# Kernel tuning notes

Measured on AMD Instinct MI355X. Metric: run time of the kernel, lower is better.

The kernel has to match this reference:

```python
import jax, jax.numpy as jnp
import numpy as np

B, S, D, H, DH, TLEN, TD = 4, 1024, 1024, 16, 64, 256, 256
EPS = 1e-5


def layer_norm(x, g, b):
    m = jnp.mean(x, axis=-1, keepdims=True)
    v = jnp.mean((x - m) ** 2, axis=-1, keepdims=True)
    return (x - m) * jax.lax.rsqrt(v + EPS) * g + b


def rotate_half(x):
    x1, x2 = jnp.split(x, 2, axis=-1)
    return jnp.concatenate((-x2, x1), axis=-1)


def apply_rope(pos, t):
    # pos: [S, DH] -> [1, S, 1, DH]; t: [B, S, H, DH]
    p = pos[None, :, None, :]
    return t * jnp.cos(p) + rotate_half(t) * jnp.sin(p)


def mha(q_in, kv_in, in_w, in_b, out_w, out_b, n_heads):
    # standard nn.MultiheadAttention math (batch-first tensors here)
    d = q_in.shape[-1]
    dh = d // n_heads
    q = q_in @ in_w[:d].T + in_b[:d]
    k = kv_in @ in_w[d:2 * d].T + in_b[d:2 * d]
    v = kv_in @ in_w[2 * d:].T + in_b[2 * d:]
    q = q.reshape(q.shape[0], q.shape[1], n_heads, dh)
    k = k.reshape(k.shape[0], k.shape[1], n_heads, dh)
    v = v.reshape(v.shape[0], v.shape[1], n_heads, dh)
    scores = jnp.einsum('bihd,bjhd->bhij', q, k) / jnp.sqrt(jnp.asarray(dh, q.dtype))
    attn = jax.nn.softmax(scores, axis=-1)
    o = jnp.einsum('bhij,bjhd->bihd', attn, v)
    o = o.reshape(o.shape[0], o.shape[1], d)
    return o @ out_w.T + out_b


def setup_inputs():
    key = jax.random.key(0)
    ks = jax.random.split(key, 20)
    s = 0.02
    inp = {
        'x': jax.random.normal(ks[0], (B, S, D), jnp.float32),
        'text_emb': jax.random.normal(ks[1], (B, TLEN, D), jnp.float32),
        'time_emb': jax.random.normal(ks[2], (B, TD), jnp.float32),
    }
    # true RoPE position encoding, matching RotaryEmbedding.forward
    inv_freq = 1.0 / (10000 ** (jnp.arange(0, DH, 2, dtype=jnp.float32) / DH))
    freqs = jnp.arange(S, dtype=jnp.float32)[:, None] * inv_freq[None, :]
    inp['rotary_pos'] = jnp.concatenate((freqs, freqs), axis=-1)  # [S, DH]
    inp.update(
        ln1_g=jnp.ones((D,), jnp.float32), ln1_b=jnp.zeros((D,), jnp.float32),
        ln2_g=jnp.ones((D,), jnp.float32), ln2_b=jnp.zeros((D,), jnp.float32),
        ln3_g=jnp.ones((D,), jnp.float32), ln3_b=jnp.zeros((D,), jnp.float32),
        attn_in_w=jax.random.normal(ks[3], (3 * D, D), jnp.float32) * s,
        attn_in_b=jnp.zeros((3 * D,), jnp.float32),
        ca_in_w=jax.random.normal(ks[4], (3 * D, D), jnp.float32) * s,
        ca_in_b=jnp.zeros((3 * D,), jnp.float32),
        ca_out_w=jax.random.normal(ks[5], (D, D), jnp.float32) * s,
        ca_out_b=jnp.zeros((D,), jnp.float32),
        fc1_w=jax.random.normal(ks[6], (4 * D, D), jnp.float32) * s,
        fc1_b=jnp.zeros((4 * D,), jnp.float32),
        gate_w=jax.random.normal(ks[7], (4 * D, D), jnp.float32) * s,
        gate_b=jnp.zeros((4 * D,), jnp.float32),
        fc2_w=jax.random.normal(ks[8], (D, 4 * D), jnp.float32) * s,
        fc2_b=jnp.zeros((D,), jnp.float32),
    )
    return inp


def reference(x, text_emb, time_emb, rotary_pos,
              ln1_g, ln1_b, ln2_g, ln2_b, ln3_g, ln3_b,
              attn_in_w, attn_in_b,
              ca_in_w, ca_in_b, ca_out_w, ca_out_b,
              fc1_w, fc1_b, gate_w, gate_b, fc2_w, fc2_b):
    b, n, d = x.shape
    # --- self-attention with manual RoPE (NOTE: original skips out_proj) ---
    residual = x
    xn = layer_norm(x, ln1_g, ln1_b)
    q = xn @ attn_in_w[:d].T + attn_in_b[:d]
    k = xn @ attn_in_w[d:2 * d].T + attn_in_b[d:2 * d]
    v = xn @ attn_in_w[2 * d:].T + attn_in_b[2 * d:]
    q = q.reshape(b, n, H, DH)
    k = k.reshape(b, n, H, DH)
    v = v.reshape(b, n, H, DH)
    q = apply_rope(rotary_pos, q)
    k = apply_rope(rotary_pos, k)
    scores = jnp.einsum('bihd,bjhd->bhij', q, k) / jnp.sqrt(jnp.asarray(DH, x.dtype))
    attn = jax.nn.softmax(scores, axis=-1)
    attn_out = jnp.einsum('bhij,bjhd->bihd', attn, v).reshape(b, n, d)
    x = attn_out + residual
    # --- cross-attention (full MHA, dropout inactive at eval) ---
    residual = x
    xn = layer_norm(x, ln2_g, ln2_b)
    x = mha(xn, text_emb, ca_in_w, ca_in_b, ca_out_w, ca_out_b, H) + residual
    # --- gated MLP ---
    residual = x
    xn = layer_norm(x, ln3_g, ln3_b)
    h = jax.nn.gelu(xn @ fc1_w.T + fc1_b, approximate=False)
    g = jax.nn.sigmoid(xn @ gate_w.T + gate_b)
    return (h * g) @ fc2_w.T + fc2_b + residual
```

## Files before the change

kernel.cpp:

```cpp
#include <hip/hip_runtime.h>
#include <hip/hip_bf16.h>

#define SEQ 1024
#define DIM 1024
#define NH 16

typedef __bf16 bf16_t;
typedef __bf16 bf16x8 __attribute__((ext_vector_type(8)));
typedef __bf16 bf16x4 __attribute__((ext_vector_type(4)));
typedef float f32x4 __attribute__((ext_vector_type(4)));

__device__ __forceinline__ f32x4 mfma16(bf16x8 a, bf16x8 b, f32x4 c) {
    return __builtin_amdgcn_mfma_f32_16x16x32_bf16(a, b, c, 0, 0, 0);
}

__device__ __forceinline__ void gload16(const bf16_t* g, bf16_t* l) {
    __builtin_amdgcn_global_load_lds(
        (const __attribute__((address_space(1))) void*)g,
        (__attribute__((address_space(3))) void*)l, 16, 0, 0);
}

enum { EPI_BF16 = 0, EPI_F32_RESID = 1 };

__global__ __launch_bounds__(256) void cvt_kernel(const float* __restrict__ in,
                                                  bf16_t* __restrict__ out) {
    const int i = blockIdx.x * 256 + threadIdx.x;
    const float4 v = ((const float4*)in)[i];
    bf16x4 o = {(bf16_t)v.x, (bf16_t)v.y, (bf16_t)v.z, (bf16_t)v.w};
    ((bf16x4*)out)[i] = o;
}

__global__ __launch_bounds__(256) void ln_kernel(const float* __restrict__ in,
                                                 const float* __restrict__ g,
                                                 const float* __restrict__ bsh,
                                                 bf16_t* __restrict__ out) {
    __shared__ float red[4], red2[4];
    const int row = blockIdx.x, tid = threadIdx.x;
    const float4 v = ((const float4*)(in + (size_t)row * DIM))[tid];
    float s = v.x + v.y + v.z + v.w;
#pragma unroll
    for (int o = 32; o; o >>= 1) s += __shfl_down(s, o, 64);
    if ((tid & 63) == 0) red[tid >> 6] = s;
    __syncthreads();
    const float mean = (red[0] + red[1] + red[2] + red[3]) * (1.0f / DIM);
    const float dx = v.x - mean, dy = v.y - mean, dz = v.z - mean, dw = v.w - mean;
    float s2 = dx * dx + dy * dy + dz * dz + dw * dw;
#pragma unroll
    for (int o = 32; o; o >>= 1) s2 += __shfl_xor(s2, o, 64);
    if ((tid & 63) == 0) red2[tid >> 6] = s2;
    __syncthreads();
    const float var = (red2[0] + red2[1] + red2[2] + red2[3]) * (1.0f / DIM);
    const float rs = rsqrtf(var + 1e-5f);
    const float4 gv = ((const float4*)g)[tid];
    const float4 bv = ((const float4*)bsh)[tid];
    bf16x4 o4 = {(bf16_t)(dx * rs * gv.x + bv.x), (bf16_t)(dy * rs * gv.y + bv.y),
                 (bf16_t)(dz * rs * gv.z + bv.z), (bf16_t)(dw * rs * gv.w + bv.w)};
    ((bf16x4*)(out + (size_t)row * DIM))[tid] = o4;
}

__global__ __launch_bounds__(256) void rope_kernel(bf16_t* __restrict__ qkv,
                                                   const float* __restrict__ rp) {
    const int t = blockIdx.x * 256 + threadIdx.x;
    const int row = t >> 9;
    const int rem = t & 511;
    const int h = rem >> 5, d = rem & 31;
    const int s = row & (SEQ - 1);
    const float p0 = rp[s * 64 + d];
    const float p1 = rp[s * 64 + d + 32];
    float s0, c0, s1, c1;
    sincosf(p0, &s0, &c0);
    sincosf(p1, &s1, &c1);
    const size_t base = (size_t)row * 3072 + h * 64 + d;
#pragma unroll
    for (int off = 0; off <= 1024; off += 1024) {
        const float a = (float)qkv[base + off];
        const float b = (float)qkv[base + off + 32];
        qkv[base + off] = (bf16_t)(a * c0 - b * s0);
        qkv[base + off + 32] = (bf16_t)(b * c1 + a * s1);
    }
}

__device__ __forceinline__ float epi_apply_gelu(float v) {
    return 0.5f * v * (1.0f + erff(v * 0.70710678118f));
}

__global__ __launch_bounds__(256) void vtrans_kernel(
    const bf16_t* __restrict__ src, int ld, int voff, int skv,
    bf16_t* __restrict__ vt) {
    __shared__ bf16_t T[64 * 72];
    const int qt = blockIdx.x, h = blockIdx.y, b = blockIdx.z;
    const int tid = threadIdx.x;
    const int s0 = qt * 64;
#pragma unroll
    for (int t = 0; t < 2; ++t) {
        const int idx = t * 256 + tid;
        const int r = idx >> 3, c8 = (idx & 7) * 8;
        bf16x8 v = *(const bf16x8*)(src + (size_t)(b * skv + s0 + r) * ld +
                                    voff + h * 64 + c8);
        *(bf16x8*)&T[r * 72 + c8] = v;
    }
    __syncthreads();
    const size_t base = ((size_t)(b * NH + h) * 64) * skv;
#pragma unroll
    for (int t = 0; t < 2; ++t) {
        const int idx = t * 256 + tid;
        const int d = idx >> 3, s8 = (idx & 7) * 8;
        bf16x8 w;
#pragma unroll
        for (int i = 0; i < 8; ++i) w[i] = T[(s8 + i) * 72 + d];
        *(bf16x8*)(vt + base + (size_t)d * skv + s0 + s8) = w;
    }
}

#define ALD 72
template <bool OUTBF>
__global__ __launch_bounds__(256) void attn2_kernel(
    const bf16_t* __restrict__ qp, int ldq, int qoff,
    const bf16_t* __restrict__ kp, int ldk, int koff,
    const bf16_t* __restrict__ vtp, int skv,
    const float* __restrict__ resid, void* __restrict__ outp, float scale) {
    __shared__ bf16_t Ks[4096];
    __shared__ bf16_t Vs[4096];
    __shared__ bf16_t Ps[4 * 16 * ALD];
    const int nwg = gridDim.x;
    const int t = (blockIdx.x & 7) * (nwg >> 3) + (blockIdx.x >> 3);
    const int qt = t & 15;
    const int bh = t >> 4;
    const int b = bh >> 4, h = bh & 15;
    const int tid = threadIdx.x;
    const int wave = tid >> 6, lane = tid & 63;
    const int lr = lane & 15, hi = lane >> 4;

    const size_t qrow = (size_t)(b * SEQ + qt * 64 + wave * 16 + lr);
    const bf16_t* qb = qp + qrow * ldq + qoff + h * 64;
    const bf16x8 qf0 = *(const bf16x8*)(qb + hi * 8);
    const bf16x8 qf1 = *(const bf16x8*)(qb + 32 + hi * 8);

    const bf16_t* vbase = vtp + ((size_t)bh * 64) * skv;

    f32x4 oacc[4];
#pragma unroll
    for (int n = 0; n < 4; ++n) oacc[n] = (f32x4){0.f, 0.f, 0.f, 0.f};
    float mrun[4] = {-1e30f, -1e30f, -1e30f, -1e30f};
    float lrun[4] = {0.f, 0.f, 0.f, 0.f};

    bf16_t* pw = &Ps[wave * 16 * ALD];
    const int nkt = skv >> 6;
    for (int kt = 0; kt < nkt; ++kt) {
#pragma unroll
        for (int u = 0; u < 2; ++u) {
            const int c = wave * 2 + u;
            const int grow = wave * 16 + lr, gcol = u * 32 + hi * 8;
            gload16(kp + (size_t)(b * skv + kt * 64 + grow) * ldk + koff +
                        h * 64 + gcol,
                    &Ks[c * 512]);
            gload16(vbase + (size_t)grow * skv + kt * 64 + gcol, &Vs[c * 512]);
        }
        __syncthreads();

        f32x4 s[4];
#pragma unroll
        for (int n = 0; n < 4; ++n) {
            f32x4 z = (f32x4){0.f, 0.f, 0.f, 0.f};
            z = mfma16(qf0, *(const bf16x8*)&Ks[(n * 2 + 0) * 512 + hi * 128 + lr * 8], z);
            z = mfma16(qf1, *(const bf16x8*)&Ks[(n * 2 + 1) * 512 + hi * 128 + lr * 8], z);
            s[n] = z * scale;
        }
        float alpha[4];
#pragma unroll
        for (int j = 0; j < 4; ++j) {
            float mt = fmaxf(fmaxf(s[0][j], s[1][j]), fmaxf(s[2][j], s[3][j]));
#pragma unroll
            for (int o = 8; o >= 1; o >>= 1) mt = fmaxf(mt, __shfl_xor(mt, o, 64));
            const float mnew = fmaxf(mrun[j], mt);
            alpha[j] = __expf(mrun[j] - mnew);
            float rsum = 0.f;
#pragma unroll
            for (int n = 0; n < 4; ++n) {
                const float p = __expf(s[n][j] - mnew);
                s[n][j] = p;
                rsum += p;
            }
#pragma unroll
            for (int o = 8; o >= 1; o >>= 1) rsum += __shfl_xor(rsum, o, 64);
            lrun[j] = lrun[j] * alpha[j] + rsum;
            mrun[j] = mnew;
        }
#pragma unroll
        for (int j = 0; j < 4; ++j) {
            const int pr = hi * 4 + j;
#pragma unroll
            for (int n = 0; n < 4; ++n) pw[pr * ALD + n * 16 + lr] = (bf16_t)s[n][j];
        }
#pragma unroll
        for (int n = 0; n < 4; ++n)
#pragma unroll
            for (int j = 0; j < 4; ++j) oacc[n][j] *= alpha[j];
#pragma unroll
        for (int ks = 0; ks < 2; ++ks) {
            const bf16x8 pa = *(const bf16x8*)&pw[lr * ALD + ks * 32 + hi * 8];
#pragma unroll
            for (int n = 0; n < 4; ++n) {
                const bf16x8 vf =
                    *(const bf16x8*)&Vs[(n * 2 + ks) * 512 + hi * 128 + lr * 8];
                oacc[n] = mfma16(pa, vf, oacc[n]);
            }
        }
        __syncthreads();
    }

    const size_t orow0 = (size_t)(b * SEQ + qt * 64 + wave * 16);
#pragma unroll
    for (int n = 0; n < 4; ++n) {
#pragma unroll
        for (int j = 0; j < 4; ++j) {
            const int r = hi * 4 + j;
            const size_t idx = (orow0 + r) * DIM + h * 64 + n * 16 + lr;
            float val = oacc[n][j] / lrun[j];
            if constexpr (OUTBF) {
                ((bf16_t*)outp)[idx] = (bf16_t)val;
            } else {
                ((float*)outp)[idx] = val + resid[idx];
            }
        }
    }
}

template <int EPI, int MODE>
__global__ __launch_bounds__(256, 3) void gemm4w(
    const bf16_t* __restrict__ A, int lda, const bf16_t* __restrict__ W, int ldw,
    const float* __restrict__ bias, const void* __restrict__ aux,
    void* __restrict__ outv, int ldo, int K, int nM) {
    __shared__ bf16_t As[2][4096];
    __shared__ bf16_t Bs[2][4096];
    const int tid = threadIdx.x;
    const int wave = tid >> 6, lane = tid & 63;
    const int wm = wave >> 1, wn = wave & 1;
    const int lr = lane & 15, hi = lane >> 4;

    const int x = blockIdx.x & 7, i = blockIdx.x >> 3;
    int mt, nt;
    if constexpr (MODE == 0) {
        const int mc = nM >> 3;
        mt = x * mc + (i % mc);
        nt = i / mc;
    } else {
        const int nc = (gridDim.x / nM) >> 3;
        nt = x * nc + (i % nc);
        mt = i / nc;
    }
    const int rowA0 = mt * 128, rowB0 = nt * 128;

    f32x4 acc[4][4];
#pragma unroll
    for (int m = 0; m < 4; ++m)
#pragma unroll
        for (int n = 0; n < 4; ++n) acc[m][n] = (f32x4){0.f, 0.f, 0.f, 0.f};

    auto stage = [&](int kt, int b) {
        const int k0 = kt * 32;
        const int gcol = k0 + hi * 8;
#pragma unroll
        for (int u = 0; u < 2; ++u) {
            const int c = wave * 2 + u;
            const int grow = c * 16 + lr;
            gload16(A + (size_t)(rowA0 + grow) * lda + gcol, &As[b][c * 512]);
            gload16(W + (size_t)(rowB0 + grow) * ldw + gcol, &Bs[b][c * 512]);
        }
    };

    const int NT = K >> 5;
    stage(0, 0);
    stage(1, 1);
    asm volatile("s_waitcnt vmcnt(4)" ::: "memory");
    __builtin_amdgcn_s_barrier();

    for (int kt = 0; kt < NT; ++kt) {
        const int cur = kt & 1;
        bf16x8 af[4], bfr[4];
#pragma unroll
        for (int mf = 0; mf < 4; ++mf)
            af[mf] = *(const bf16x8*)&As[cur][(wm * 4 + mf) * 512 + hi * 128 + lr * 8];
#pragma unroll
        for (int nf = 0; nf < 4; ++nf)
            bfr[nf] = *(const bf16x8*)&Bs[cur][(wn * 4 + nf) * 512 + hi * 128 + lr * 8];
#pragma unroll
        for (int mf = 0; mf < 4; ++mf)
#pragma unroll
            for (int nf = 0; nf < 4; ++nf)
                acc[mf][nf] = mfma16(af[mf], bfr[nf], acc[mf][nf]);
        if (kt + 1 < NT) {
            __builtin_amdgcn_sched_barrier(0);
            __builtin_amdgcn_s_barrier();
            if (kt + 2 < NT) {
                stage(kt + 2, cur);
                asm volatile("s_waitcnt vmcnt(4)" ::: "memory");
            } else {
                asm volatile("s_waitcnt vmcnt(0)" ::: "memory");
            }
            __builtin_amdgcn_s_barrier();
        }
    }

    float bn[4];
#pragma unroll
    for (int n = 0; n < 4; ++n) bn[n] = bias[rowB0 + wn * 64 + n * 16 + lr];
#pragma unroll
    for (int m = 0; m < 4; ++m) {
#pragma unroll
        for (int j = 0; j < 4; ++j) {
            const int row = rowA0 + wm * 64 + m * 16 + hi * 4 + j;
#pragma unroll
            for (int n = 0; n < 4; ++n) {
                const int col = rowB0 + wn * 64 + n * 16 + lr;
                float val = acc[m][n][j] + bn[n];
                const size_t oidx = (size_t)row * ldo + col;
                if constexpr (EPI == EPI_BF16) {
                    ((bf16_t*)outv)[oidx] = (bf16_t)val;
                } else {
                    ((float*)outv)[oidx] = val + ((const float*)aux)[oidx];
                }
            }
        }
    }
}

__global__ __launch_bounds__(256, 3) void gemm_mlp(
    const bf16_t* __restrict__ A, int lda, const bf16_t* __restrict__ W1,
    const bf16_t* __restrict__ Wg, int ldw, const float* __restrict__ b1,
    const float* __restrict__ bg, bf16_t* __restrict__ outv, int ldo, int K,
    int nM) {
    __shared__ __align__(16) char smem[32768];
    auto As = (bf16_t(*)[4096])smem;
    auto Bs = (bf16_t(*)[4096])(smem + 16384);
    float* gx = (float*)smem;
    const int tid = threadIdx.x;
    const int wave = tid >> 6, lane = tid & 63;
    const int role = wave >> 1, wm = wave & 1;
    const int lr = lane & 15, hi = lane >> 4;

    const int x = blockIdx.x & 7, i = blockIdx.x >> 3;
    const int nc = (gridDim.x / nM) >> 3;
    const int nt = x * nc + (i % nc), mt = i / nc;
    const int rowA0 = mt * 128, colB0 = nt * 64;

    f32x4 acc[4][4];
#pragma unroll
    for (int m = 0; m < 4; ++m)
#pragma unroll
        for (int n = 0; n < 4; ++n) acc[m][n] = (f32x4){0.f, 0.f, 0.f, 0.f};

    auto stage = [&](int kt, int b) {
        const int k0 = kt * 32;
        const int gcol = k0 + hi * 8;
#pragma unroll
        for (int u = 0; u < 2; ++u) {
            const int c = wave * 2 + u;
            gload16(A + (size_t)(rowA0 + c * 16 + lr) * lda + gcol, &As[b][c * 512]);
            const bf16_t* Wsrc = (c < 4) ? W1 : Wg;
            const int wrow = colB0 + (c & 3) * 16 + lr;
            gload16(Wsrc + (size_t)wrow * ldw + gcol, &Bs[b][c * 512]);
        }
    };

    const int NT = K >> 5;
    stage(0, 0);
    stage(1, 1);
    asm volatile("s_waitcnt vmcnt(4)" ::: "memory");
    __builtin_amdgcn_s_barrier();

    for (int kt = 0; kt < NT; ++kt) {
        const int cur = kt & 1;
        bf16x8 af[4], bfr[4];
#pragma unroll
        for (int mf = 0; mf < 4; ++mf)
            af[mf] = *(const bf16x8*)&As[cur][(wm * 4 + mf) * 512 + hi * 128 + lr * 8];
#pragma unroll
        for (int nf = 0; nf < 4; ++nf)
            bfr[nf] = *(const bf16x8*)&Bs[cur][(role * 4 + nf) * 512 + hi * 128 + lr * 8];
#pragma unroll
        for (int mf = 0; mf < 4; ++mf)
#pragma unroll
            for (int nf = 0; nf < 4; ++nf)
                acc[mf][nf] = mfma16(af[mf], bfr[nf], acc[mf][nf]);
        if (kt + 1 < NT) {
            __builtin_amdgcn_sched_barrier(0);
            __builtin_amdgcn_s_barrier();
            if (kt + 2 < NT) {
                stage(kt + 2, cur);
                asm volatile("s_waitcnt vmcnt(4)" ::: "memory");
            } else {
                asm volatile("s_waitcnt vmcnt(0)" ::: "memory");
            }
            __builtin_amdgcn_s_barrier();
        }
    }

    __syncthreads();
    if (role == 1) {
#pragma unroll
        for (int m = 0; m < 4; ++m)
#pragma unroll
            for (int j = 0; j < 4; ++j) {
                const int r = wm * 64 + m * 16 + hi * 4 + j;
#pragma unroll
                for (int n = 0; n < 4; ++n)
                    gx[r * 64 + n * 16 + lr] =
                        acc[m][n][j] + bg[colB0 + n * 16 + lr];
            }
    }
    __syncthreads();
    if (role == 0) {
#pragma unroll
        for (int m = 0; m < 4; ++m) {
#pragma unroll
            for (int j = 0; j < 4; ++j) {
                const int r = wm * 64 + m * 16 + hi * 4 + j;
                const int row = rowA0 + r;
#pragma unroll
                for (int n = 0; n < 4; ++n) {
                    const int col = colB0 + n * 16 + lr;
                    const float h = acc[m][n][j] + b1[col];
                    const float g = gx[r * 64 + n * 16 + lr];
                    const float sg = 1.0f / (1.0f + __expf(-g));
                    outv[(size_t)row * ldo + col] = (bf16_t)(epi_apply_gelu(h) * sg);
                }
            }
        }
    }
}

extern "C" void kernel_launch(void* const* d_in, const int* in_sizes, int n_in,
                              void* d_out, int out_size, void* d_ws, size_t ws_size,
                              hipStream_t stream) {
    const float* x = (const float*)d_in[0];
    const float* text_emb = (const float*)d_in[1];
    const float* rotary = (const float*)d_in[3];
    const float* ln1_g = (const float*)d_in[4];
    const float* ln1_b = (const float*)d_in[5];
    const float* ln2_g = (const float*)d_in[6];
    const float* ln2_b = (const float*)d_in[7];
    const float* ln3_g = (const float*)d_in[8];
    const float* ln3_b = (const float*)d_in[9];
    const float* attn_in_w = (const float*)d_in[10];
    const float* attn_in_b = (const float*)d_in[11];
    const float* ca_in_w = (const float*)d_in[12];
    const float* ca_in_b = (const float*)d_in[13];
    const float* ca_out_w = (const float*)d_in[14];
    const float* ca_out_b = (const float*)d_in[15];
    const float* fc1_w = (const float*)d_in[16];
    const float* fc1_b = (const float*)d_in[17];
    const float* gate_w = (const float*)d_in[18];
    const float* gate_b = (const float*)d_in[19];
    const float* fc2_w = (const float*)d_in[20];
    const float* fc2_b = (const float*)d_in[21];

    char* ws = (char*)d_ws;
    bf16_t* attn_w_bf = (bf16_t*)(ws);
    bf16_t* ca_in_bf = (bf16_t*)(ws + 6291456);
    bf16_t* ca_out_bf = (bf16_t*)(ws + 12582912);
    bf16_t* fc1_bf = (bf16_t*)(ws + 14680064);
    bf16_t* gate_bf = (bf16_t*)(ws + 23068672);
    bf16_t* fc2_bf = (bf16_t*)(ws + 31457280);
    bf16_t* text_bf = (bf16_t*)(ws + 39845888);
    bf16_t* xn = (bf16_t*)(ws + 41943040);
    float* xA = (float*)(ws + 50331648);
    char* S = ws + 67108864;
    bf16_t* qkv = (bf16_t*)S;
    bf16_t* vtSelf = (bf16_t*)(S + 25165824);
    bf16_t* cq = (bf16_t*)S;
    bf16_t* ckv = (bf16_t*)(S + 8388608);
    bf16_t* ca_attn = (bf16_t*)(S + 12582912);
    bf16_t* vtCross = (bf16_t*)(S + 20971520);
    bf16_t* hbuf = (bf16_t*)S;
    float* out = (float*)d_out;

    cvt_kernel<<<3072, 256, 0, stream>>>(attn_in_w, attn_w_bf);
    cvt_kernel<<<3072, 256, 0, stream>>>(ca_in_w, ca_in_bf);
    cvt_kernel<<<1024, 256, 0, stream>>>(ca_out_w, ca_out_bf);
    cvt_kernel<<<4096, 256, 0, stream>>>(fc1_w, fc1_bf);
    cvt_kernel<<<4096, 256, 0, stream>>>(gate_w, gate_bf);
    cvt_kernel<<<4096, 256, 0, stream>>>(fc2_w, fc2_bf);
    cvt_kernel<<<1024, 256, 0, stream>>>(text_emb, text_bf);

    ln_kernel<<<4096, 256, 0, stream>>>(x, ln1_g, ln1_b, xn);
    gemm4w<EPI_BF16, 0><<<768, 256, 0, stream>>>(
        xn, 1024, attn_w_bf, 1024, attn_in_b, nullptr, qkv, 3072, 1024, 32);
    rope_kernel<<<8192, 256, 0, stream>>>(qkv, rotary);
    vtrans_kernel<<<dim3(16, 16, 4), 256, 0, stream>>>(qkv, 3072, 2048, 1024, vtSelf);
    attn2_kernel<false><<<1024, 256, 0, stream>>>(
        qkv, 3072, 0, qkv, 3072, 1024, vtSelf, 1024, x, xA, 0.125f);

    ln_kernel<<<4096, 256, 0, stream>>>(xA, ln2_g, ln2_b, xn);
    gemm4w<EPI_BF16, 0><<<256, 256, 0, stream>>>(
        xn, 1024, ca_in_bf, 1024, ca_in_b, nullptr, cq, 1024, 1024, 32);
    gemm4w<EPI_BF16, 1><<<128, 256, 0, stream>>>(
        text_bf, 1024, ca_in_bf + (size_t)1024 * 1024, 1024, ca_in_b + 1024, nullptr,
        ckv, 2048, 1024, 8);
    vtrans_kernel<<<dim3(4, 16, 4), 256, 0, stream>>>(ckv, 2048, 1024, 256, vtCross);
    attn2_kernel<true><<<1024, 256, 0, stream>>>(
        cq, 1024, 0, ckv, 2048, 0, vtCross, 256, nullptr, ca_attn, 0.125f);
    gemm4w<EPI_F32_RESID, 0><<<256, 256, 0, stream>>>(
        ca_attn, 1024, ca_out_bf, 1024, ca_out_b, xA, xA, 1024, 1024, 32);

    ln_kernel<<<4096, 256, 0, stream>>>(xA, ln3_g, ln3_b, xn);
    gemm_mlp<<<2048, 256, 0, stream>>>(
        xn, 1024, fc1_bf, gate_bf, 1024, fc1_b, gate_b, hbuf, 4096, 1024, 32);
    gemm4w<EPI_F32_RESID, 0><<<256, 256, 0, stream>>>(
        hbuf, 4096, fc2_bf, 4096, fc2_b, xA, out, 1024, 4096, 32);
}
```

Before: 527.6 us.

## Add 256x256-tile 8-wave GEMM and use it for QKV and MLP projections

Introduces a 512-thread GEMM kernel with 256x256 output tiles, BK=64 double-buffered LDS staging, and an MFMA schedule split into four quadrants, with interleaved barriers and setprio. It replaces the QKV projection GEMM and splits the fused fc1/gate GEMM into two launches: a GELU epilogue, then a sigmoid-multiply epilogue that reads the stored bf16 h back in place. The larger tiles are meant to raise arithmetic intensity and cut global traffic per FLOP. In exchange, the MLP path writes and re-reads the hidden buffer, h is rounded to bf16 before the multiply, and the grids get smaller (192/256 blocks), which may leave CUs underused.

```diff
diff --git a/kernel.cpp b/kernel.cpp
--- a/kernel.cpp
+++ b/kernel.cpp
@@ -20,7 +20,7 @@
         (__attribute__((address_space(3))) void*)l, 16, 0, 0);
 }
 
-enum { EPI_BF16 = 0, EPI_F32_RESID = 1 };
+enum { EPI_BF16 = 0, EPI_F32_RESID = 1, EPI_BF16_GELU = 2, EPI_BF16_SIGMUL = 3 };
 
 __global__ __launch_bounds__(256) void cvt_kernel(const float* __restrict__ in,
                                                   bf16_t* __restrict__ out) {
@@ -226,6 +226,175 @@
     }
 }
 
+template <int EPI>
+__global__ __launch_bounds__(512, 2) void gemm8p(
+    const bf16_t* __restrict__ A, int lda, const bf16_t* __restrict__ W, int ldw,
+    const float* __restrict__ bias, const void* __restrict__ aux,
+    void* __restrict__ outv, int ldo, int K, int nM) {
+    __shared__ bf16_t As[2][16384];
+    __shared__ bf16_t Bs[2][16384];
+    const int tid = threadIdx.x;
+    const int wave = tid >> 6, lane = tid & 63;
+    const int wm = wave >> 2, wn = wave & 3;
+    const int lr = lane & 15, hi = lane >> 4;
+
+    const int x = blockIdx.x & 7, i = blockIdx.x >> 3;
+    const int mc = nM >> 3;
+    const int mt = x * mc + (i % mc);
+    const int nt = i / mc;
+    const int rowA0 = mt * 256, rowB0 = nt * 256;
+
+    f32x4 acc[8][4];
+#pragma unroll
+    for (int m = 0; m < 8; ++m)
+#pragma unroll
+        for (int n = 0; n < 4; ++n) acc[m][n] = (f32x4){0.f, 0.f, 0.f, 0.f};
+
+    auto stageA = [&](int kt, int b) {
+        const int k0 = kt * 64;
+#pragma unroll
+        for (int h2 = 0; h2 < 2; ++h2)
+#pragma unroll
+            for (int u = 0; u < 2; ++u) {
+                const int c = wave * 2 + u;
+                const int grow = rowA0 + h2 * 128 + (c >> 1) * 16 + lr;
+                const int gcol = k0 + (c & 1) * 32 + hi * 8;
+                gload16(A + (size_t)grow * lda + gcol, &As[b][h2 * 8192 + c * 512]);
+            }
+    };
+    auto stageB = [&](int kt, int b) {
+        const int k0 = kt * 64;
+#pragma unroll
+        for (int h2 = 0; h2 < 2; ++h2)
+#pragma unroll
+            for (int u = 0; u < 2; ++u) {
+                const int c = wave * 2 + u;
+                const int grow = rowB0 + h2 * 128 + (c >> 1) * 16 + lr;
+                const int gcol = k0 + (c & 1) * 32 + hi * 8;
+                gload16(W + (size_t)grow * ldw + gcol, &Bs[b][h2 * 8192 + c * 512]);
+            }
+    };
+
+    const int NT = K >> 6;
+    stageA(0, 0);
+    stageB(0, 0);
+    stageA(1, 1);
+    stageB(1, 1);
+    asm volatile("s_waitcnt vmcnt(8)" ::: "memory");
+    __builtin_amdgcn_s_barrier();
+
+    for (int kt = 0; kt < NT; ++kt) {
+        const int cur = kt & 1;
+        const bf16_t* Ab = &As[cur][wm * 8192];
+        const bf16_t* Bb = &Bs[cur][(wn >> 1) * 8192 + (wn & 1) * 4096];
+        bf16x8 af[4][2], bflo[2][2], bfhi[2][2];
+
+#pragma unroll
+        for (int mf = 0; mf < 4; ++mf)
+#pragma unroll
+            for (int ks = 0; ks < 2; ++ks)
+                af[mf][ks] = *(const bf16x8*)&Ab[(mf * 2 + ks) * 512 + lane * 8];
+#pragma unroll
+        for (int nf = 0; nf < 2; ++nf)
+#pragma unroll
+            for (int ks = 0; ks < 2; ++ks)
+                bflo[nf][ks] = *(const bf16x8*)&Bb[(nf * 2 + ks) * 512 + lane * 8];
+        __builtin_amdgcn_s_barrier();
+        __builtin_amdgcn_s_setprio(1);
+#pragma unroll
+        for (int mf = 0; mf < 4; ++mf)
+#pragma unroll
+            for (int nf = 0; nf < 2; ++nf)
+#pragma unroll
+                for (int ks = 0; ks < 2; ++ks)
+                    acc[mf][nf] = mfma16(af[mf][ks], bflo[nf][ks], acc[mf][nf]);
+        __builtin_amdgcn_s_setprio(0);
+        __builtin_amdgcn_s_barrier();
+
+#pragma unroll
+        for (int nf = 0; nf < 2; ++nf)
+#pragma unroll
+            for (int ks = 0; ks < 2; ++ks)
+                bfhi[nf][ks] = *(const bf16x8*)&Bb[((nf + 2) * 2 + ks) * 512 + lane * 8];
+        __builtin_amdgcn_s_barrier();
+        __builtin_amdgcn_s_setprio(1);
+#pragma unroll
+        for (int mf = 0; mf < 4; ++mf)
+#pragma unroll
+            for (int nf = 0; nf < 2; ++nf)
+#pragma unroll
+                for (int ks = 0; ks < 2; ++ks)
+                    acc[mf][nf + 2] = mfma16(af[mf][ks], bfhi[nf][ks], acc[mf][nf + 2]);
+        __builtin_amdgcn_s_setprio(0);
+        __builtin_amdgcn_s_barrier();
+
+#pragma unroll
+        for (int mf = 0; mf < 4; ++mf)
+#pragma unroll
+            for (int ks = 0; ks < 2; ++ks)
+                af[mf][ks] = *(const bf16x8*)&Ab[((mf + 4) * 2 + ks) * 512 + lane * 8];
+        if (kt + 2 < NT) stageB(kt + 2, cur);
+        __builtin_amdgcn_s_barrier();
+        __builtin_amdgcn_s_setprio(1);
+#pragma unroll
+        for (int mf = 0; mf < 4; ++mf)
+#pragma unroll
+            for (int nf = 0; nf < 2; ++nf)
+#pragma unroll
+                for (int ks = 0; ks < 2; ++ks)
+                    acc[mf + 4][nf + 2] = mfma16(af[mf][ks], bfhi[nf][ks], acc[mf + 4][nf + 2]);
+        __builtin_amdgcn_s_setprio(0);
+        __builtin_amdgcn_s_barrier();
+
+        if (kt + 2 < NT) stageA(kt + 2, cur);
+        __builtin_amdgcn_s_barrier();
+        __builtin_amdgcn_s_setprio(1);
+#pragma unroll
+        for (int mf = 0; mf < 4; ++mf)
+#pragma unroll
+            for (int nf = 0; nf < 2; ++nf)
+#pragma unroll
+                for (int ks = 0; ks < 2; ++ks)
+                    acc[mf + 4][nf] = mfma16(af[mf][ks], bflo[nf][ks], acc[mf + 4][nf]);
+        __builtin_amdgcn_s_setprio(0);
+        if (kt + 1 < NT) {
+            if (kt + 2 < NT)
+                asm volatile("s_waitcnt vmcnt(8)" ::: "memory");
+            else
+                asm volatile("s_waitcnt vmcnt(0)" ::: "memory");
+            __builtin_amdgcn_s_barrier();
+        }
+    }
+
+    float bn[4];
+#pragma unroll
+    for (int n = 0; n < 4; ++n) bn[n] = bias[rowB0 + wn * 64 + n * 16 + lr];
+#pragma unroll
+    for (int m = 0; m < 8; ++m) {
+#pragma unroll
+        for (int j = 0; j < 4; ++j) {
+            const int row = rowA0 + wm * 128 + m * 16 + hi * 4 + j;
+#pragma unroll
+            for (int n = 0; n < 4; ++n) {
+                const int col = rowB0 + wn * 64 + n * 16 + lr;
+                float val = acc[m][n][j] + bn[n];
+                const size_t oidx = (size_t)row * ldo + col;
+                if constexpr (EPI == EPI_BF16) {
+                    ((bf16_t*)outv)[oidx] = (bf16_t)val;
+                } else if constexpr (EPI == EPI_BF16_GELU) {
+                    ((bf16_t*)outv)[oidx] = (bf16_t)epi_apply_gelu(val);
+                } else if constexpr (EPI == EPI_BF16_SIGMUL) {
+                    const float sg = 1.0f / (1.0f + __expf(-val));
+                    ((bf16_t*)outv)[oidx] =
+                        (bf16_t)(sg * (float)((const bf16_t*)aux)[oidx]);
+                } else {
+                    ((float*)outv)[oidx] = val + ((const float*)aux)[oidx];
+                }
+            }
+        }
+    }
+}
+
 template <int EPI, int MODE>
 __global__ __launch_bounds__(256, 3) void gemm4w(
     const bf16_t* __restrict__ A, int lda, const bf16_t* __restrict__ W, int ldw,
@@ -319,111 +488,6 @@
                     ((bf16_t*)outv)[oidx] = (bf16_t)val;
                 } else {
                     ((float*)outv)[oidx] = val + ((const float*)aux)[oidx];
-                }
-            }
-        }
-    }
-}
-
-__global__ __launch_bounds__(256, 3) void gemm_mlp(
-    const bf16_t* __restrict__ A, int lda, const bf16_t* __restrict__ W1,
-    const bf16_t* __restrict__ Wg, int ldw, const float* __restrict__ b1,
-    const float* __restrict__ bg, bf16_t* __restrict__ outv, int ldo, int K,
-    int nM) {
-    __shared__ __align__(16) char smem[32768];
-    auto As = (bf16_t(*)[4096])smem;
-    auto Bs = (bf16_t(*)[4096])(smem + 16384);
-    float* gx = (float*)smem;
-    const int tid = threadIdx.x;
-    const int wave = tid >> 6, lane = tid & 63;
-    const int role = wave >> 1, wm = wave & 1;
-    const int lr = lane & 15, hi = lane >> 4;
-
-    const int x = blockIdx.x & 7, i = blockIdx.x >> 3;
-    const int nc = (gridDim.x / nM) >> 3;
-    const int nt = x * nc + (i % nc), mt = i / nc;
-    const int rowA0 = mt * 128, colB0 = nt * 64;
-
-    f32x4 acc[4][4];
-#pragma unroll
-    for (int m = 0; m < 4; ++m)
-#pragma unroll
-        for (int n = 0; n < 4; ++n) acc[m][n] = (f32x4){0.f, 0.f, 0.f, 0.f};
-
-    auto stage = [&](int kt, int b) {
-        const int k0 = kt * 32;
-        const int gcol = k0 + hi * 8;
-#pragma unroll
-        for (int u = 0; u < 2; ++u) {
-            const int c = wave * 2 + u;
-            gload16(A + (size_t)(rowA0 + c * 16 + lr) * lda + gcol, &As[b][c * 512]);
-            const bf16_t* Wsrc = (c < 4) ? W1 : Wg;
-            const int wrow = colB0 + (c & 3) * 16 + lr;
-            gload16(Wsrc + (size_t)wrow * ldw + gcol, &Bs[b][c * 512]);
-        }
-    };
-
-    const int NT = K >> 5;
-    stage(0, 0);
-    stage(1, 1);
-    asm volatile("s_waitcnt vmcnt(4)" ::: "memory");
-    __builtin_amdgcn_s_barrier();
-
-    for (int kt = 0; kt < NT; ++kt) {
-        const int cur = kt & 1;
-        bf16x8 af[4], bfr[4];
-#pragma unroll
-        for (int mf = 0; mf < 4; ++mf)
-            af[mf] = *(const bf16x8*)&As[cur][(wm * 4 + mf) * 512 + hi * 128 + lr * 8];
-#pragma unroll
-        for (int nf = 0; nf < 4; ++nf)
-            bfr[nf] = *(const bf16x8*)&Bs[cur][(role * 4 + nf) * 512 + hi * 128 + lr * 8];
-#pragma unroll
-        for (int mf = 0; mf < 4; ++mf)
-#pragma unroll
-            for (int nf = 0; nf < 4; ++nf)
-                acc[mf][nf] = mfma16(af[mf], bfr[nf], acc[mf][nf]);
-        if (kt + 1 < NT) {
-            __builtin_amdgcn_sched_barrier(0);
-            __builtin_amdgcn_s_barrier();
-            if (kt + 2 < NT) {
-                stage(kt + 2, cur);
-                asm volatile("s_waitcnt vmcnt(4)" ::: "memory");
-            } else {
-                asm volatile("s_waitcnt vmcnt(0)" ::: "memory");
-            }
-            __builtin_amdgcn_s_barrier();
-        }
-    }
-
-    __syncthreads();
-    if (role == 1) {
-#pragma unroll
-        for (int m = 0; m < 4; ++m)
-#pragma unroll
-            for (int j = 0; j < 4; ++j) {
-                const int r = wm * 64 + m * 16 + hi * 4 + j;
-#pragma unroll
-                for (int n = 0; n < 4; ++n)
-                    gx[r * 64 + n * 16 + lr] =
-                        acc[m][n][j] + bg[colB0 + n * 16 + lr];
-            }
-    }
-    __syncthreads();
-    if (role == 0) {
-#pragma unroll
-        for (int m = 0; m < 4; ++m) {
-#pragma unroll
-            for (int j = 0; j < 4; ++j) {
-                const int r = wm * 64 + m * 16 + hi * 4 + j;
-                const int row = rowA0 + r;
-#pragma unroll
-                for (int n = 0; n < 4; ++n) {
-                    const int col = colB0 + n * 16 + lr;
-                    const float h = acc[m][n][j] + b1[col];
-                    const float g = gx[r * 64 + n * 16 + lr];
-                    const float sg = 1.0f / (1.0f + __expf(-g));
-                    outv[(size_t)row * ldo + col] = (bf16_t)(epi_apply_gelu(h) * sg);
                 }
             }
         }
@@ -484,8 +548,8 @@
     cvt_kernel<<<1024, 256, 0, stream>>>(text_emb, text_bf);
 
     ln_kernel<<<4096, 256, 0, stream>>>(x, ln1_g, ln1_b, xn);
-    gemm4w<EPI_BF16, 0><<<768, 256, 0, stream>>>(
-        xn, 1024, attn_w_bf, 1024, attn_in_b, nullptr, qkv, 3072, 1024, 32);
+    gemm8p<EPI_BF16><<<192, 512, 0, stream>>>(
+        xn, 1024, attn_w_bf, 1024, attn_in_b, nullptr, qkv, 3072, 1024, 16);
     rope_kernel<<<8192, 256, 0, stream>>>(qkv, rotary);
     vtrans_kernel<<<dim3(16, 16, 4), 256, 0, stream>>>(qkv, 3072, 2048, 1024, vtSelf);
     attn2_kernel<false><<<1024, 256, 0, stream>>>(
@@ -504,8 +568,10 @@
         ca_attn, 1024, ca_out_bf, 1024, ca_out_b, xA, xA, 1024, 1024, 32);
 
     ln_kernel<<<4096, 256, 0, stream>>>(xA, ln3_g, ln3_b, xn);
-    gemm_mlp<<<2048, 256, 0, stream>>>(
-        xn, 1024, fc1_bf, gate_bf, 1024, fc1_b, gate_b, hbuf, 4096, 1024, 32);
+    gemm8p<EPI_BF16_GELU><<<256, 512, 0, stream>>>(
+        xn, 1024, fc1_bf, 1024, fc1_b, nullptr, hbuf, 4096, 1024, 16);
+    gemm8p<EPI_BF16_SIGMUL><<<256, 512, 0, stream>>>(
+        xn, 1024, gate_bf, 1024, gate_b, hbuf, hbuf, 4096, 1024, 16);
     gemm4w<EPI_F32_RESID, 0><<<256, 256, 0, stream>>>(
         hbuf, 4096, fc2_bf, 4096, fc2_b, xA, out, 1024, 4096, 32);
 }
```

After: 602.5 us. +14.2%, slower.
